# Kernel optimization log

Hardware: AMD Instinct MI355X
Metric: run time of the kernel (lower is better)

The kernel has to match this reference:

```python
import jax, jax.numpy as jnp
import numpy as np
import math

N_HEADS = 16
D_MODEL = 1024
HEAD_DIM = D_MODEL // N_HEADS
ROPE_THETA = 10000.0


def _rope_cos_sin(seq_len, head_dim, dtype):
    # freqs = 1/theta^(2i/d), angles = outer(t, freqs)  -> [seq_len, head_dim//2]
    inv_freq = 1.0 / (ROPE_THETA ** (jnp.arange(0, head_dim, 2, dtype=jnp.float32) / head_dim))
    ang = jnp.arange(seq_len, dtype=jnp.float32)[:, None] * inv_freq[None, :]
    return jnp.cos(ang).astype(dtype), jnp.sin(ang).astype(dtype)


def _apply_rope(t, cos, sin):
    # t: [B, N, H, D]; treat last dim as complex pairs (a, b); multiply by e^{i*ang}
    B, N, H, D = t.shape
    tr = t.reshape(B, N, H, D // 2, 2)
    a, b = tr[..., 0], tr[..., 1]
    c = cos[None, :, None, :]  # [1, N, 1, D/2]
    s = sin[None, :, None, :]
    out = jnp.stack([a * c - b * s, a * s + b * c], axis=-1)
    return out.reshape(B, N, H, D)


def setup_inputs() -> dict:
    key = jax.random.key(0)
    ks = jax.random.split(key, 9)
    B, N, D = 4, 2048, D_MODEL
    scale = 0.02
    inp = {"x": jax.random.normal(ks[0], (B, N, D), dtype=jnp.float32)}
    for i, nm in enumerate(["q", "k", "v", "o"]):
        inp[f"w{nm}"] = jax.random.normal(ks[1 + 2 * i], (D, D), dtype=jnp.float32) * scale
        inp[f"b{nm}"] = jax.random.normal(ks[2 + 2 * i], (D,), dtype=jnp.float32) * scale
    return inp


def reference(x, wq, bq, wk, bk, wv, bv, wo, bo):
    B, N, D = x.shape
    H, Hd = N_HEADS, HEAD_DIM
    q = (x @ wq.T + bq).reshape(B, N, H, Hd)
    k = (x @ wk.T + bk).reshape(B, N, H, Hd)
    v = (x @ wv.T + bv).reshape(B, N, H, Hd)
    cos, sin = _rope_cos_sin(N, Hd, x.dtype)
    q = _apply_rope(q, cos, sin)
    k = _apply_rope(k, cos, sin)
    # SDPA, no mask, eval mode (dropout_p = 0)
    scores = jnp.einsum("bqhd,bkhd->bhqk", q, k) / math.sqrt(Hd)
    attn = jax.nn.softmax(scores, axis=-1)
    out = jnp.einsum("bhqk,bkhd->bqhd", attn, v)  # [B, N, H, Hd]
    out = out.reshape(B, N, D)
    return out @ wo.T + bo
```

## Files before the change

### kernel.cpp

```cpp
#include <hip/hip_runtime.h>
#include <math.h>
#include <stdint.h>

#define BBATCH 4
#define NTOK   2048
#define DMOD   1024
#define NH     16
#define HD     64
#define MTOT   8192

typedef __bf16 bf16;
typedef __bf16 bf16x4 __attribute__((ext_vector_type(4)));
typedef __bf16 bf16x8 __attribute__((ext_vector_type(8)));
typedef float  f32x4  __attribute__((ext_vector_type(4)));

typedef __attribute__((address_space(3))) unsigned int lds_u32;
typedef __attribute__((address_space(1))) unsigned int glb_u32;

__device__ __forceinline__ void gload16(const bf16* g, bf16* l) {
    __builtin_amdgcn_global_load_lds((glb_u32*)g, (lds_u32*)l, 16, 0, 0);
}

__global__ void rope_table_kernel(float* __restrict__ ct, float* __restrict__ st) {
    int idx = blockIdx.x * 256 + threadIdx.x;
    if (idx >= NTOK * 32) return;
    int n = idx >> 5, p = idx & 31;
    float inv = powf(10000.0f, -(float)(2 * p) / 64.0f);
    float ang = (float)n * inv;
    ct[idx] = cosf(ang);
    st[idx] = sinf(ang);
}

__global__ __launch_bounds__(256)
void convert_kernel(const float* __restrict__ x,  const float* __restrict__ wq,
                    const float* __restrict__ wk, const float* __restrict__ wv,
                    const float* __restrict__ wo,
                    bf16* __restrict__ xb,  bf16* __restrict__ wqb,
                    bf16* __restrict__ wkb, bf16* __restrict__ wvb,
                    bf16* __restrict__ wob)
{
    const int X4 = (MTOT * DMOD) / 4;
    const int W4 = (DMOD * DMOD) / 4;
    int i = blockIdx.x * 256 + threadIdx.x;
    const float* src; bf16* dst; int off;
    if (i < X4) { src = x; dst = xb; off = i; }
    else {
        int j = i - X4; int w = j / W4; off = j - w * W4;
        src = (w == 0) ? wq : (w == 1) ? wk : (w == 2) ? wv : wo;
        dst = (w == 0) ? wqb : (w == 1) ? wkb : (w == 2) ? wvb : wob;
    }
    float4 v = ((const float4*)src)[off];
    bf16x4 o;
    o[0] = (bf16)v.x; o[1] = (bf16)v.y; o[2] = (bf16)v.z; o[3] = (bf16)v.w;
    *(bf16x4*)(dst + (size_t)off * 4) = o;
}

template <int MODE>
__global__ __launch_bounds__(256)
void gemm_mfma(const bf16* __restrict__ A, const bf16* __restrict__ W,
               const float* __restrict__ bias, void* __restrict__ outv,
               const float* __restrict__ ct, const float* __restrict__ st)
{
    __shared__ __align__(16) bf16 As[128 * 32];
    __shared__ __align__(16) bf16 Bs[128 * 32];

    const int tid = threadIdx.x;
    const int l   = tid & 63;
    const int wid = tid >> 6;
    const int wm  = wid >> 1, wn = wid & 1;
    const int fr  = l & 15, fg = l >> 4;
    const int m0 = blockIdx.y * 128, n0 = blockIdx.x * 128;

    const int srow  = tid >> 2;
    const int sslot = (tid & 3) ^ ((srow >> 1) & 3);
    const bf16* gA0 = A + (size_t)(m0 + srow) * 1024 + sslot * 8;
    const bf16* gB0 = W + (size_t)(n0 + srow) * 1024 + sslot * 8;
    bf16* lA0 = As + tid * 8;
    bf16* lA1 = As + 2048 + tid * 8;
    bf16* lB0 = Bs + tid * 8;
    bf16* lB1 = Bs + 2048 + tid * 8;

    const int aswz = (fg ^ ((fr >> 1) & 3)) * 8;
    const bf16* ap[4]; const bf16* bp[4];
#pragma unroll
    for (int i = 0; i < 4; ++i) {
        ap[i] = As + (wm * 64 + i * 16 + fr) * 32 + aswz;
        bp[i] = Bs + (wn * 64 + i * 16 + fr) * 32 + aswz;
    }

    f32x4 acc[4][4] = {};

    for (int kt = 0; kt < 32; ++kt) {
        __syncthreads();
        const bf16* a0 = gA0 + kt * 32;
        const bf16* b0 = gB0 + kt * 32;
        gload16(a0, lA0);
        gload16(a0 + (size_t)64 * 1024, lA1);
        gload16(b0, lB0);
        gload16(b0 + (size_t)64 * 1024, lB1);
        __syncthreads();

        bf16x8 af[4], bfv[4];
#pragma unroll
        for (int i = 0; i < 4; ++i) af[i]  = *(const bf16x8*)ap[i];
#pragma unroll
        for (int i = 0; i < 4; ++i) bfv[i] = *(const bf16x8*)bp[i];
#pragma unroll
        for (int mi = 0; mi < 4; ++mi)
#pragma unroll
            for (int ni = 0; ni < 4; ++ni)
                acc[mi][ni] = __builtin_amdgcn_mfma_f32_16x16x32_bf16(
                    af[mi], bfv[ni], acc[mi][ni], 0, 0, 0);
    }

    if (MODE == 0) {
        float* out = (float*)outv;
#pragma unroll
        for (int ni = 0; ni < 4; ++ni) {
            const int col = n0 + wn * 64 + ni * 16 + fr;
            const float bv = bias[col];
#pragma unroll
            for (int mi = 0; mi < 4; ++mi) {
                const int rowb = m0 + wm * 64 + mi * 16 + fg * 4;
#pragma unroll
                for (int r = 0; r < 4; ++r)
                    out[(size_t)(rowb + r) * 1024 + col] = acc[mi][ni][r] + bv;
            }
        }
    } else if (MODE == 3) {
        bf16* out = (bf16*)outv;
#pragma unroll
        for (int ni = 0; ni < 4; ++ni) {
            const int col = n0 + wn * 64 + ni * 16 + fr;
            const int h = col >> 6, dd = col & 63;
            const float bv = bias[col];
#pragma unroll
            for (int mi = 0; mi < 4; ++mi) {
                const int rowb = m0 + wm * 64 + mi * 16 + fg * 4;
                const int bi = rowb >> 11, npb = rowb & (NTOK - 1);
                bf16x4 ov;
#pragma unroll
                for (int r = 0; r < 4; ++r) ov[r] = (bf16)(acc[mi][ni][r] + bv);
                *(bf16x4*)(out + ((size_t)(bi * NH + h) * HD + dd) * NTOK + npb) = ov;
            }
        }
    } else {
        bf16* out = (bf16*)outv;
#pragma unroll
        for (int ni = 0; ni < 4; ++ni) {
            const int col = n0 + wn * 64 + ni * 16 + fr;
            const int h = col >> 6, dd = col & 63, p = (dd >> 1);
            const float bv = bias[col];
#pragma unroll
            for (int mi = 0; mi < 4; ++mi) {
                const int rowb = m0 + wm * 64 + mi * 16 + fg * 4;
#pragma unroll
                for (int r = 0; r < 4; ++r) {
                    const int row = rowb + r;
                    const int bi = row >> 11, np = row & (NTOK - 1);
                    float v  = acc[mi][ni][r] + bv;
                    float pv = __shfl_xor(v, 1);
                    float c = ct[np * 32 + p], s = st[np * 32 + p];
                    float o = (dd & 1) ? (pv * s + v * c) : (v * c - pv * s);
                    if (MODE == 1) o *= 0.125f;
                    out[((size_t)(bi * NH + h) * NTOK + np) * HD + dd] = (bf16)o;
                }
            }
        }
    }
}

__global__ __launch_bounds__(256)
void attn_mfma(const bf16* __restrict__ Q, const bf16* __restrict__ K,
               const bf16* __restrict__ Vt, bf16* __restrict__ out)
{
    __shared__ __align__(16) bf16 Ks[64 * 64];
    __shared__ __align__(16) bf16 Vs[64 * 64];
    __shared__ __align__(16) bf16 Ps[4 * 32 * 64];

    const int tid = threadIdx.x;
    const int l   = tid & 63;
    const int wid = tid >> 6;
    const int fr  = l & 15, fg = l >> 4;
    const int q0 = blockIdx.x * 128;
    const int bh = blockIdx.y;

    const bf16* Qb = Q  + (size_t)bh * NTOK * HD;
    const bf16* Kb = K  + (size_t)bh * NTOK * HD;
    const bf16* Vb = Vt + (size_t)bh * HD * NTOK;
    bf16* Pw = Ps + wid * (32 * 64);

    bf16x8 qf[2][2];
#pragma unroll
    for (int nq = 0; nq < 2; ++nq)
#pragma unroll
        for (int ks = 0; ks < 2; ++ks)
            qf[nq][ks] = *(const bf16x8*)(Qb + (size_t)(q0 + wid * 32 + nq * 16 + fr) * HD
                                          + ks * 32 + fg * 8);

    const int srow  = tid >> 3;
    const int sslot = (tid & 7) ^ (srow & 7);
    const bf16* gK0 = Kb + (size_t)srow * HD + sslot * 8;
    const bf16* gV0 = Vb + (size_t)srow * NTOK + sslot * 8;
    bf16* lK0 = Ks + tid * 8;
    bf16* lK1 = Ks + 2048 + tid * 8;
    bf16* lV0 = Vs + tid * 8;
    bf16* lV1 = Vs + 2048 + tid * 8;

    float m_i[2] = { -INFINITY, -INFINITY };
    float l_i[2] = { 0.f, 0.f };
    f32x4 o[4][2] = {};

    for (int t = 0; t < 32; ++t) {
        __syncthreads();
        const bf16* gK = gK0 + (size_t)t * 64 * HD;
        const bf16* gV = gV0 + (size_t)t * 64;
        gload16(gK, lK0);
        gload16(gK + 32 * HD, lK1);
        gload16(gV, lV0);
        gload16(gV + (size_t)32 * NTOK, lV1);
        __syncthreads();

        f32x4 tt[4][2] = {};
#pragma unroll
        for (int ks = 0; ks < 2; ++ks) {
            bf16x8 kf[4];
#pragma unroll
            for (int mk = 0; mk < 4; ++mk)
                kf[mk] = *(const bf16x8*)(Ks + (mk * 16 + fr) * 64
                                          + (((ks * 4 + fg) ^ (fr & 7)) * 8));
#pragma unroll
            for (int mk = 0; mk < 4; ++mk)
#pragma unroll
                for (int nq = 0; nq < 2; ++nq)
                    tt[mk][nq] = __builtin_amdgcn_mfma_f32_16x16x32_bf16(
                        kf[mk], qf[nq][ks], tt[mk][nq], 0, 0, 0);
        }

#pragma unroll
        for (int nq = 0; nq < 2; ++nq) {
            float mx = -INFINITY;
#pragma unroll
            for (int mk = 0; mk < 4; ++mk)
#pragma unroll
                for (int r = 0; r < 4; ++r) mx = fmaxf(mx, tt[mk][nq][r]);
            mx = fmaxf(mx, __shfl_xor(mx, 16));
            mx = fmaxf(mx, __shfl_xor(mx, 32));
            const float mn   = fmaxf(m_i[nq], mx);
            const float corr = __expf(m_i[nq] - mn);
            m_i[nq] = mn;
            float rs = 0.f;
#pragma unroll
            for (int mk = 0; mk < 4; ++mk)
#pragma unroll
                for (int r = 0; r < 4; ++r) {
                    float p = __expf(tt[mk][nq][r] - mn);
                    tt[mk][nq][r] = p; rs += p;
                }
            rs += __shfl_xor(rs, 16);
            rs += __shfl_xor(rs, 32);
            l_i[nq] = l_i[nq] * corr + rs;
#pragma unroll
            for (int md = 0; md < 4; ++md) o[md][nq] *= corr;
#pragma unroll
            for (int mk = 0; mk < 4; ++mk) {
                bf16x4 pk;
#pragma unroll
                for (int r = 0; r < 4; ++r) pk[r] = (bf16)tt[mk][nq][r];
                *(bf16x4*)(Pw + (nq * 16 + fr) * 64
                           + (((2 * mk + (fg >> 1)) ^ (fr & 7)) * 8) + (fg & 1) * 4) = pk;
            }
        }

#pragma unroll
        for (int ks = 0; ks < 2; ++ks) {
            bf16x8 vf[4], pf[2];
#pragma unroll
            for (int md = 0; md < 4; ++md)
                vf[md] = *(const bf16x8*)(Vs + (md * 16 + fr) * 64
                                          + (((ks * 4 + fg) ^ (fr & 7)) * 8));
#pragma unroll
            for (int nq = 0; nq < 2; ++nq)
                pf[nq] = *(const bf16x8*)(Pw + (nq * 16 + fr) * 64
                                          + (((ks * 4 + fg) ^ (fr & 7)) * 8));
#pragma unroll
            for (int md = 0; md < 4; ++md)
#pragma unroll
                for (int nq = 0; nq < 2; ++nq)
                    o[md][nq] = __builtin_amdgcn_mfma_f32_16x16x32_bf16(
                        vf[md], pf[nq], o[md][nq], 0, 0, 0);
        }
    }

    const int b_ = bh >> 4, h = bh & 15;
#pragma unroll
    for (int nq = 0; nq < 2; ++nq) {
        const float inv = 1.0f / l_i[nq];
        const int token = q0 + wid * 32 + nq * 16 + fr;
#pragma unroll
        for (int md = 0; md < 4; ++md) {
            bf16x4 ov;
#pragma unroll
            for (int r = 0; r < 4; ++r) ov[r] = (bf16)(o[md][nq][r] * inv);
            *(bf16x4*)(out + (size_t)(b_ * NTOK + token) * DMOD + h * HD + md * 16 + fg * 4) = ov;
        }
    }
}

extern "C" void kernel_launch(void* const* d_in, const int* in_sizes, int n_in,
                              void* d_out, int out_size, void* d_ws, size_t ws_size,
                              hipStream_t stream)
{
    (void)in_sizes; (void)n_in; (void)out_size; (void)ws_size;

    const float* x  = (const float*)d_in[0];
    const float* wq = (const float*)d_in[1];
    const float* bq = (const float*)d_in[2];
    const float* wk = (const float*)d_in[3];
    const float* bk = (const float*)d_in[4];
    const float* wv = (const float*)d_in[5];
    const float* bv = (const float*)d_in[6];
    const float* wo = (const float*)d_in[7];
    const float* bo = (const float*)d_in[8];
    float* out = (float*)d_out;

    const size_t XSZ = (size_t)MTOT * DMOD;
    const size_t WSZ = (size_t)DMOD * DMOD;
    bf16* xb  = (bf16*)d_ws;
    bf16* wqb = xb  + XSZ;
    bf16* wkb = wqb + WSZ;
    bf16* wvb = wkb + WSZ;
    bf16* wob = wvb + WSZ;
    bf16* qb  = wob + WSZ;
    bf16* kb  = qb  + XSZ;
    bf16* vtb = kb  + XSZ;
    bf16* ab  = vtb + XSZ;
    float* ct = (float*)(ab + XSZ);
    float* st = ct + (size_t)NTOK * 32;

    rope_table_kernel<<<dim3(256), dim3(256), 0, stream>>>(ct, st);
    convert_kernel<<<dim3(12288), dim3(256), 0, stream>>>(x, wq, wk, wv, wo,
                                                          xb, wqb, wkb, wvb, wob);

    dim3 gg(DMOD / 128, MTOT / 128);
    gemm_mfma<1><<<gg, dim3(256), 0, stream>>>(xb, wqb, bq, qb,  ct, st);
    gemm_mfma<2><<<gg, dim3(256), 0, stream>>>(xb, wkb, bk, kb,  ct, st);
    gemm_mfma<3><<<gg, dim3(256), 0, stream>>>(xb, wvb, bv, vtb, ct, st);

    attn_mfma<<<dim3(NTOK / 128, BBATCH * NH), dim3(256), 0, stream>>>(qb, kb, vtb, ab);

    gemm_mfma<0><<<gg, dim3(256), 0, stream>>>(ab, wob, bo, out, ct, st);
}
```

Baseline: 366.0 us.

## Double-buffer LDS tiles in GEMM and attention, use exp2 with lazy rescaling

Both the projection GEMM and the attention kernel now keep two shared-memory buffers and issue the next tile's global-to-LDS loads before computing on the current tile. This drops one barrier per iteration and lets memory latency overlap with MFMA work. The attention softmax now works in base 2: log2(e) is folded into the Q scale, exp2 replaces expf, and the running-max rescale is skipped unless the max grows by more than 8 for some lane. That cuts exponentials and multiplies, at the cost of more LDS per block and the risk of larger intermediate values before the rescale happens.

After: 359.6 us. No clear change (-1.7%).

```diff
diff --git a/kernel.cpp b/kernel.cpp
--- a/kernel.cpp
+++ b/kernel.cpp
@@ -20,6 +20,8 @@
 __device__ __forceinline__ void gload16(const bf16* g, bf16* l) {
     __builtin_amdgcn_global_load_lds((glb_u32*)g, (lds_u32*)l, 16, 0, 0);
 }
+
+#define QSCALE 0.1803368801111204f
 
 __global__ void rope_table_kernel(float* __restrict__ ct, float* __restrict__ st) {
     int idx = blockIdx.x * 256 + threadIdx.x;
@@ -61,8 +63,8 @@
                const float* __restrict__ bias, void* __restrict__ outv,
                const float* __restrict__ ct, const float* __restrict__ st)
 {
-    __shared__ __align__(16) bf16 As[128 * 32];
-    __shared__ __align__(16) bf16 Bs[128 * 32];
+    __shared__ __align__(16) bf16 As[2][128 * 32];
+    __shared__ __align__(16) bf16 Bs[2][128 * 32];
 
     const int tid = threadIdx.x;
     const int l   = tid & 63;
@@ -75,43 +77,49 @@
     const int sslot = (tid & 3) ^ ((srow >> 1) & 3);
     const bf16* gA0 = A + (size_t)(m0 + srow) * 1024 + sslot * 8;
     const bf16* gB0 = W + (size_t)(n0 + srow) * 1024 + sslot * 8;
-    bf16* lA0 = As + tid * 8;
-    bf16* lA1 = As + 2048 + tid * 8;
-    bf16* lB0 = Bs + tid * 8;
-    bf16* lB1 = Bs + 2048 + tid * 8;
 
     const int aswz = (fg ^ ((fr >> 1) & 3)) * 8;
-    const bf16* ap[4]; const bf16* bp[4];
+    int aoff[4], boff[4];
 #pragma unroll
     for (int i = 0; i < 4; ++i) {
-        ap[i] = As + (wm * 64 + i * 16 + fr) * 32 + aswz;
-        bp[i] = Bs + (wn * 64 + i * 16 + fr) * 32 + aswz;
+        aoff[i] = (wm * 64 + i * 16 + fr) * 32 + aswz;
+        boff[i] = (wn * 64 + i * 16 + fr) * 32 + aswz;
     }
 
     f32x4 acc[4][4] = {};
 
+#define GSTAGE(kt, b) do {                                   \
+        const bf16* a0_ = gA0 + (kt) * 32;                   \
+        const bf16* b0_ = gB0 + (kt) * 32;                   \
+        gload16(a0_,                      As[b] + tid * 8);  \
+        gload16(a0_ + (size_t)64 * 1024,  As[b] + 2048 + tid * 8); \
+        gload16(b0_,                      Bs[b] + tid * 8);  \
+        gload16(b0_ + (size_t)64 * 1024,  Bs[b] + 2048 + tid * 8); \
+    } while (0)
+
+    GSTAGE(0, 0);
+    __syncthreads();
+    int cur = 0;
+
     for (int kt = 0; kt < 32; ++kt) {
-        __syncthreads();
-        const bf16* a0 = gA0 + kt * 32;
-        const bf16* b0 = gB0 + kt * 32;
-        gload16(a0, lA0);
-        gload16(a0 + (size_t)64 * 1024, lA1);
-        gload16(b0, lB0);
-        gload16(b0 + (size_t)64 * 1024, lB1);
-        __syncthreads();
+        if (kt < 31) GSTAGE(kt + 1, cur ^ 1);
 
         bf16x8 af[4], bfv[4];
 #pragma unroll
-        for (int i = 0; i < 4; ++i) af[i]  = *(const bf16x8*)ap[i];
-#pragma unroll
-        for (int i = 0; i < 4; ++i) bfv[i] = *(const bf16x8*)bp[i];
+        for (int i = 0; i < 4; ++i) af[i]  = *(const bf16x8*)(As[cur] + aoff[i]);
+#pragma unroll
+        for (int i = 0; i < 4; ++i) bfv[i] = *(const bf16x8*)(Bs[cur] + boff[i]);
 #pragma unroll
         for (int mi = 0; mi < 4; ++mi)
 #pragma unroll
             for (int ni = 0; ni < 4; ++ni)
                 acc[mi][ni] = __builtin_amdgcn_mfma_f32_16x16x32_bf16(
                     af[mi], bfv[ni], acc[mi][ni], 0, 0, 0);
-    }
+
+        __syncthreads();
+        cur ^= 1;
+    }
+#undef GSTAGE
 
     if (MODE == 0) {
         float* out = (float*)outv;
@@ -162,7 +170,7 @@
                     float pv = __shfl_xor(v, 1);
                     float c = ct[np * 32 + p], s = st[np * 32 + p];
                     float o = (dd & 1) ? (pv * s + v * c) : (v * c - pv * s);
-                    if (MODE == 1) o *= 0.125f;
+                    if (MODE == 1) o *= QSCALE;
                     out[((size_t)(bi * NH + h) * NTOK + np) * HD + dd] = (bf16)o;
                 }
             }
@@ -174,9 +182,9 @@
 void attn_mfma(const bf16* __restrict__ Q, const bf16* __restrict__ K,
                const bf16* __restrict__ Vt, bf16* __restrict__ out)
 {
-    __shared__ __align__(16) bf16 Ks[64 * 64];
-    __shared__ __align__(16) bf16 Vs[64 * 64];
-    __shared__ __align__(16) bf16 Ps[4 * 32 * 64];
+    __shared__ __align__(16) bf16 Ks[2][64 * 64];
+    __shared__ __align__(16) bf16 Vs[2][64 * 64];
+    __shared__ __align__(16) bf16 Ps[4][32 * 64];
 
     const int tid = threadIdx.x;
     const int l   = tid & 63;
@@ -188,7 +196,7 @@
     const bf16* Qb = Q  + (size_t)bh * NTOK * HD;
     const bf16* Kb = K  + (size_t)bh * NTOK * HD;
     const bf16* Vb = Vt + (size_t)bh * HD * NTOK;
-    bf16* Pw = Ps + wid * (32 * 64);
+    bf16* Pw = Ps[wid];
 
     bf16x8 qf[2][2];
 #pragma unroll
@@ -202,24 +210,28 @@
     const int sslot = (tid & 7) ^ (srow & 7);
     const bf16* gK0 = Kb + (size_t)srow * HD + sslot * 8;
     const bf16* gV0 = Vb + (size_t)srow * NTOK + sslot * 8;
-    bf16* lK0 = Ks + tid * 8;
-    bf16* lK1 = Ks + 2048 + tid * 8;
-    bf16* lV0 = Vs + tid * 8;
-    bf16* lV1 = Vs + 2048 + tid * 8;
+
+#define ASTAGE(t, b) do {                                        \
+        const bf16* gK_ = gK0 + (size_t)(t) * 64 * HD;           \
+        const bf16* gV_ = gV0 + (size_t)(t) * 64;                \
+        gload16(gK_,                      Ks[b] + tid * 8);      \
+        gload16(gK_ + 32 * HD,            Ks[b] + 2048 + tid * 8); \
+        gload16(gV_,                      Vs[b] + tid * 8);      \
+        gload16(gV_ + (size_t)32 * NTOK,  Vs[b] + 2048 + tid * 8); \
+    } while (0)
 
     float m_i[2] = { -INFINITY, -INFINITY };
     float l_i[2] = { 0.f, 0.f };
     f32x4 o[4][2] = {};
 
+    ASTAGE(0, 0);
+    __syncthreads();
+    int cur = 0;
+
     for (int t = 0; t < 32; ++t) {
-        __syncthreads();
-        const bf16* gK = gK0 + (size_t)t * 64 * HD;
-        const bf16* gV = gV0 + (size_t)t * 64;
-        gload16(gK, lK0);
-        gload16(gK + 32 * HD, lK1);
-        gload16(gV, lV0);
-        gload16(gV + (size_t)32 * NTOK, lV1);
-        __syncthreads();
+        if (t < 31) ASTAGE(t + 1, cur ^ 1);
+        const bf16* Kc = Ks[cur];
+        const bf16* Vc = Vs[cur];
 
         f32x4 tt[4][2] = {};
 #pragma unroll
@@ -227,7 +239,7 @@
             bf16x8 kf[4];
 #pragma unroll
             for (int mk = 0; mk < 4; ++mk)
-                kf[mk] = *(const bf16x8*)(Ks + (mk * 16 + fr) * 64
+                kf[mk] = *(const bf16x8*)(Kc + (mk * 16 + fr) * 64
                                           + (((ks * 4 + fg) ^ (fr & 7)) * 8));
 #pragma unroll
             for (int mk = 0; mk < 4; ++mk)
@@ -239,29 +251,32 @@
 
 #pragma unroll
         for (int nq = 0; nq < 2; ++nq) {
-            float mx = -INFINITY;
+            float pmax = -INFINITY;
 #pragma unroll
             for (int mk = 0; mk < 4; ++mk)
 #pragma unroll
-                for (int r = 0; r < 4; ++r) mx = fmaxf(mx, tt[mk][nq][r]);
-            mx = fmaxf(mx, __shfl_xor(mx, 16));
-            mx = fmaxf(mx, __shfl_xor(mx, 32));
-            const float mn   = fmaxf(m_i[nq], mx);
-            const float corr = __expf(m_i[nq] - mn);
-            m_i[nq] = mn;
+                for (int r = 0; r < 4; ++r) pmax = fmaxf(pmax, tt[mk][nq][r]);
+            pmax = fmaxf(pmax, __shfl_xor(pmax, 16));
+            pmax = fmaxf(pmax, __shfl_xor(pmax, 32));
+            if (!__all(pmax - m_i[nq] <= 8.0f)) {
+                const float mn   = fmaxf(m_i[nq], pmax);
+                const float corr = __builtin_amdgcn_exp2f(m_i[nq] - mn);
+                l_i[nq] *= corr;
+#pragma unroll
+                for (int md = 0; md < 4; ++md) o[md][nq] *= corr;
+                m_i[nq] = mn;
+            }
             float rs = 0.f;
 #pragma unroll
             for (int mk = 0; mk < 4; ++mk)
 #pragma unroll
                 for (int r = 0; r < 4; ++r) {
-                    float p = __expf(tt[mk][nq][r] - mn);
+                    float p = __builtin_amdgcn_exp2f(tt[mk][nq][r] - m_i[nq]);
                     tt[mk][nq][r] = p; rs += p;
                 }
             rs += __shfl_xor(rs, 16);
             rs += __shfl_xor(rs, 32);
-            l_i[nq] = l_i[nq] * corr + rs;
-#pragma unroll
-            for (int md = 0; md < 4; ++md) o[md][nq] *= corr;
+            l_i[nq] += rs;
 #pragma unroll
             for (int mk = 0; mk < 4; ++mk) {
                 bf16x4 pk;
@@ -277,7 +292,7 @@
             bf16x8 vf[4], pf[2];
 #pragma unroll
             for (int md = 0; md < 4; ++md)
-                vf[md] = *(const bf16x8*)(Vs + (md * 16 + fr) * 64
+                vf[md] = *(const bf16x8*)(Vc + (md * 16 + fr) * 64
                                           + (((ks * 4 + fg) ^ (fr & 7)) * 8));
 #pragma unroll
             for (int nq = 0; nq < 2; ++nq)
@@ -290,7 +305,11 @@
                     o[md][nq] = __builtin_amdgcn_mfma_f32_16x16x32_bf16(
                         vf[md], pf[nq], o[md][nq], 0, 0, 0);
         }
-    }
+
+        __syncthreads();
+        cur ^= 1;
+    }
+#undef ASTAGE
 
     const int b_ = bh >> 4, h = bh & 15;
 #pragma unroll
```
